# Kernel optimization log

Measured on AMD Instinct MI355X. Metric: run time of the kernel, lower is better.

The kernel has to match this reference:

```python
import jax, jax.numpy as jnp
import numpy as np

D = 1024      # model_dim (input_dim)
H = 2048      # hidden_size_per_expert (hardcoded in module)
E = 8         # num_experts
K = 2         # topk
T = 8192      # tokens (batch after view)


def setup_inputs() -> dict:
    key = jax.random.key(0)
    ks = jax.random.split(key, 6)
    s_in = 1.0 / np.sqrt(D)
    s_h = 1.0 / np.sqrt(H)
    return {
        "x": jax.random.normal(ks[0], (T, D), dtype=jnp.float32),
        "wg": jax.random.normal(ks[1], (D, E), dtype=jnp.float32) * s_in,   # gate Linear(D,E,bias=False)
        "w1": jax.random.normal(ks[2], (E, D, H), dtype=jnp.float32) * s_in,
        "b1": jnp.zeros((E, H), dtype=jnp.float32),
        "w2": jax.random.normal(ks[3], (E, H, D), dtype=jnp.float32) * s_h,
        "b2": jnp.zeros((E, D), dtype=jnp.float32),
    }


def _moe(x, wg, w1, b1, w2, b2):
    # top-k gating (Tutel 'top' gate, k=K)
    logits = x @ wg                         # [T,E]
    scores = jax.nn.softmax(logits, -1)     # [T,E]
    topv, topi = jax.lax.top_k(scores, K)   # [T,K]
    sel = jax.nn.one_hot(topi, E, dtype=x.dtype)          # [T,K,E]
    combine = jnp.einsum('tk,tke->te', topv, sel)          # sparse combine weights [T,E]
    # GShard-style load-balance aux loss (top-1 dispatch mask)
    ce = sel[:, 0, :].mean(0)               # fraction of tokens whose top1 is e
    me = scores.mean(0)                     # mean gate prob per expert
    l_aux = jnp.sum(me * ce) * E
    # expert FFN (dense over experts; combine zeros out non-selected)
    h = jax.nn.relu(jnp.einsum('td,edh->teh', x, w1) + b1)  # [T,E,H]
    y = jnp.einsum('teh,ehd->ted', h, w2) + b2              # [T,E,D]
    out = jnp.einsum('te,ted->td', combine, y)              # [T,D]
    return out, l_aux


def reference(x, wg, w1, b1, w2, b2):
    return _moe(x, wg, w1, b1, w2, b2)
```

## Files before the change

### kernel.cpp

```cpp
#include <hip/hip_runtime.h>
#include <stdint.h>

#define T_TOK 8192
#define DIM   1024
#define HID   2048
#define NE    8

#define BM 128
#define BN 128
#define BK 64

#define GB_TOK 32

typedef float floatx4 __attribute__((ext_vector_type(4)));
typedef short shortx8 __attribute__((ext_vector_type(8)));

typedef __attribute__((address_space(3))) void       lds_void;
typedef const __attribute__((address_space(1))) void gbl_void;

__device__ __forceinline__ unsigned short f2bf(float f) {
  unsigned int u = __float_as_uint(f);
  unsigned int r = 0x7fffu + ((u >> 16) & 1u);
  return (unsigned short)((u + r) >> 16);
}

__global__ __launch_bounds__(256) void transpose_cast_kernel(const float* __restrict__ in,
                                                             unsigned short* __restrict__ out,
                                                             int R, int C) {
  __shared__ float tile[32][33];
  const size_t eoff = (size_t)blockIdx.z * R * C;
  const float* ip = in + eoff;
  unsigned short* op = out + eoff;
  int c0 = blockIdx.x * 32, r0 = blockIdx.y * 32;
  int tx = threadIdx.x, ty = threadIdx.y;
#pragma unroll
  for (int i = 0; i < 4; i++)
    tile[ty + i * 8][tx] = ip[(size_t)(r0 + ty + i * 8) * C + (c0 + tx)];
  __syncthreads();
#pragma unroll
  for (int i = 0; i < 4; i++)
    op[(size_t)(c0 + ty + i * 8) * R + (r0 + tx)] = f2bf(tile[tx][ty + i * 8]);
}

__global__ __launch_bounds__(256) void gate_kernel(const float* __restrict__ x,
                                                   const float* __restrict__ wg,
                                                   unsigned short* __restrict__ xb,
                                                   int* counts, int* top1cnt, float* ssum,
                                                   int* tok_list, float* wgt_list) {
  __shared__ int   lds_cnt[8];
  __shared__ int   lds_top1[8];
  __shared__ float lds_ssum[4][8];
  __shared__ int   tk_e[GB_TOK][2];
  __shared__ int   tk_r[GB_TOK][2];
  __shared__ float tk_w[GB_TOK][2];
  __shared__ int   base[8];

  const int tid = threadIdx.x;
  const int wave = tid >> 6;
  const int lane = tid & 63;

  if (tid < 8) { lds_cnt[tid] = 0; lds_top1[tid] = 0; }
  if (tid < 32) lds_ssum[tid >> 3][tid & 7] = 0.f;
  __syncthreads();

  float ssum_local[8];
#pragma unroll
  for (int e = 0; e < 8; e++) ssum_local[e] = 0.f;

  for (int it = 0; it < GB_TOK / 4; it++) {
    const int lt = it * 4 + wave;
    const int t = blockIdx.x * GB_TOK + lt;

    float acc[8];
#pragma unroll
    for (int e = 0; e < 8; e++) acc[e] = 0.f;
    const float* xr = x + (size_t)t * DIM;
    unsigned short* xw = xb + (size_t)t * DIM;
#pragma unroll
    for (int i = 0; i < 16; i++) {
      int d = i * 64 + lane;
      float xv = xr[d];
      xw[d] = f2bf(xv);
      const float4* wr = reinterpret_cast<const float4*>(wg + d * 8);
      float4 w0 = wr[0], w1 = wr[1];
      acc[0] += xv * w0.x; acc[1] += xv * w0.y; acc[2] += xv * w0.z; acc[3] += xv * w0.w;
      acc[4] += xv * w1.x; acc[5] += xv * w1.y; acc[6] += xv * w1.z; acc[7] += xv * w1.w;
    }
#pragma unroll
    for (int e = 0; e < 8; e++) {
#pragma unroll
      for (int off = 32; off > 0; off >>= 1) acc[e] += __shfl_xor(acc[e], off, 64);
    }
    if (lane == 0) {
      float mx = acc[0];
#pragma unroll
      for (int e = 1; e < 8; e++) mx = fmaxf(mx, acc[e]);
      float s[8], sum = 0.f;
#pragma unroll
      for (int e = 0; e < 8; e++) { s[e] = expf(acc[e] - mx); sum += s[e]; }
      float inv = 1.f / sum;
#pragma unroll
      for (int e = 0; e < 8; e++) { s[e] *= inv; ssum_local[e] += s[e]; }
      int i1 = 0;
#pragma unroll
      for (int e = 1; e < 8; e++) if (s[e] > s[i1]) i1 = e;
      int i2 = (i1 == 0) ? 1 : 0;
#pragma unroll
      for (int e = 0; e < 8; e++) if (e != i1 && s[e] > s[i2]) i2 = e;
      atomicAdd(&lds_top1[i1], 1);
      int r1 = atomicAdd(&lds_cnt[i1], 1);
      int r2 = atomicAdd(&lds_cnt[i2], 1);
      tk_e[lt][0] = i1; tk_r[lt][0] = r1; tk_w[lt][0] = s[i1];
      tk_e[lt][1] = i2; tk_r[lt][1] = r2; tk_w[lt][1] = s[i2];
    }
  }
  if (lane == 0) {
#pragma unroll
    for (int e = 0; e < 8; e++) lds_ssum[wave][e] = ssum_local[e];
  }
  __syncthreads();
  if (tid < 8) {
    base[tid] = atomicAdd(&counts[tid], lds_cnt[tid]);
    atomicAdd(&top1cnt[tid], lds_top1[tid]);
    atomicAdd(&ssum[tid],
              lds_ssum[0][tid] + lds_ssum[1][tid] + lds_ssum[2][tid] + lds_ssum[3][tid]);
  }
  __syncthreads();
  if (tid < GB_TOK * 2) {
    int lt = tid >> 1, k = tid & 1;
    int e = tk_e[lt][k];
    int pos = base[e] + tk_r[lt][k];
    tok_list[e * T_TOK + pos] = blockIdx.x * GB_TOK + lt;
    wgt_list[e * T_TOK + pos] = tk_w[lt][k];
  }
}

__global__ void scan_kernel(const int* counts, const int* top1cnt, const float* ssum,
                            int* h_off, int* tile_off, float* laux_out) {
  if (threadIdx.x == 0 && blockIdx.x == 0) {
    int off = 0, toff = 0;
    float l = 0.f;
    for (int e = 0; e < 8; e++) {
      h_off[e] = off;
      tile_off[e] = toff;
      off += counts[e];
      toff += (counts[e] + BM - 1) / BM;
      l += (ssum[e] / (float)T_TOK) * ((float)top1cnt[e] / (float)T_TOK);
    }
    tile_off[8] = toff;
    *laux_out = l * (float)NE;
  }
}

template <int MODE>
__global__ __launch_bounds__(256, 2) void moe_gemm_kernel(
    const unsigned short* __restrict__ A_src, const unsigned short* __restrict__ B_src,
    const float* __restrict__ bias, const int* __restrict__ counts,
    const int* __restrict__ h_off, const int* __restrict__ tile_off,
    const int* __restrict__ tok_list, const float* __restrict__ wgt_list,
    unsigned short* __restrict__ h_out, float* __restrict__ out, int N, int K) {
  __shared__ unsigned short s_a[2][BM][BK];
  __shared__ unsigned short s_b[2][BN][BK];

  const int bt = blockIdx.y;
  if (bt >= tile_off[8]) return;
  int e = 7;
#pragma unroll
  for (int q = 6; q >= 0; q--)
    if (bt < tile_off[q + 1]) e = q;
  const int n_e = counts[e];
  const int m0 = (bt - tile_off[e]) * BM;
  const int n0 = blockIdx.x * BN;
  const int tid = threadIdx.x;

  const int lane = tid & 63;
  const int wv = tid >> 6;
  const int lrow = lane >> 3;
  const int lchk = (lane & 7) ^ lrow;

  const unsigned short* a_g[4];
  const unsigned short* b_g[4];
#pragma unroll
  for (int c = 0; c < 4; c++) {
    int ra = wv * 32 + c * 8 + lrow;
    int gr = m0 + ra;
    int safe = (gr < n_e) ? gr : (n_e - 1);
    const unsigned short* abase;
    if (MODE == 0) {
      int tok = tok_list[e * T_TOK + safe];
      abase = A_src + (size_t)tok * K;
    } else {
      abase = A_src + (size_t)(h_off[e] + safe) * K;
    }
    a_g[c] = abase + lchk * 8;
    b_g[c] = B_src + ((size_t)e * N + n0 + ra) * K + lchk * 8;
  }

  auto STAGE = [&](int buf, int kt) {
#pragma unroll
    for (int c = 0; c < 4; c++) {
      __builtin_amdgcn_global_load_lds((gbl_void*)(a_g[c] + kt),
                                       (lds_void*)&s_a[buf][wv * 32 + c * 8][0], 16, 0, 0);
      __builtin_amdgcn_global_load_lds((gbl_void*)(b_g[c] + kt),
                                       (lds_void*)&s_b[buf][wv * 32 + c * 8][0], 16, 0, 0);
    }
  };

  const int lm = lane & 15;
  const int quad = lane >> 4;
  const int r7 = lm & 7;
  const int wm = (wv >> 1) * 64;
  const int wn = (wv & 1) * 64;

  floatx4 acc[4][4];
#pragma unroll
  for (int mi = 0; mi < 4; mi++)
#pragma unroll
    for (int ni = 0; ni < 4; ni++) acc[mi][ni] = (floatx4){0.f, 0.f, 0.f, 0.f};

  const int NT = K / BK;
  STAGE(0, 0);
  __syncthreads();

  int cur = 0;
  for (int t = 0; t < NT; ++t) {
    if (t + 1 < NT) STAGE(cur ^ 1, (t + 1) * BK);
#pragma unroll
    for (int kk = 0; kk < 2; kk++) {
      const int pc = ((kk << 2) + quad) ^ r7;
      shortx8 af[4], bfr[4];
#pragma unroll
      for (int mi = 0; mi < 4; mi++)
        af[mi] = *reinterpret_cast<const shortx8*>(&s_a[cur][wm + mi * 16 + lm][pc << 3]);
#pragma unroll
      for (int ni = 0; ni < 4; ni++)
        bfr[ni] = *reinterpret_cast<const shortx8*>(&s_b[cur][wn + ni * 16 + lm][pc << 3]);
#pragma unroll
      for (int mi = 0; mi < 4; mi++)
#pragma unroll
        for (int ni = 0; ni < 4; ni++)
          acc[mi][ni] = __builtin_amdgcn_mfma_f32_16x16x32_bf16(af[mi], bfr[ni], acc[mi][ni], 0, 0, 0);
    }
    __syncthreads();
    cur ^= 1;
  }

#pragma unroll
  for (int mi = 0; mi < 4; mi++) {
#pragma unroll
    for (int r = 0; r < 4; r++) {
      int row = m0 + wm + mi * 16 + quad * 4 + r;
      if (row >= n_e) continue;
      if (MODE == 0) {
        size_t base = (size_t)(h_off[e] + row) * N;
#pragma unroll
        for (int ni = 0; ni < 4; ni++) {
          int col = n0 + wn + ni * 16 + lm;
          float v = acc[mi][ni][r] + bias[e * N + col];
          v = fmaxf(v, 0.f);
          h_out[base + col] = f2bf(v);
        }
      } else {
        int tok = tok_list[e * T_TOK + row];
        float wgt = wgt_list[e * T_TOK + row];
        size_t base = (size_t)tok * N;
#pragma unroll
        for (int ni = 0; ni < 4; ni++) {
          int col = n0 + wn + ni * 16 + lm;
          float v = wgt * (acc[mi][ni][r] + bias[e * N + col]);
          atomicAdd(&out[base + col], v);
        }
      }
    }
  }
}

extern "C" void kernel_launch(void* const* d_in, const int* in_sizes, int n_in,
                              void* d_out, int out_size, void* d_ws, size_t ws_size,
                              hipStream_t stream) {
  const float* x  = (const float*)d_in[0];
  const float* wg = (const float*)d_in[1];
  const float* w1 = (const float*)d_in[2];
  const float* b1 = (const float*)d_in[3];
  const float* w2 = (const float*)d_in[4];
  const float* b2 = (const float*)d_in[5];
  float* out = (float*)d_out;

  char* ws = (char*)d_ws;
  int*            counts   = (int*)(ws + 0);
  int*            top1cnt  = (int*)(ws + 32);
  float*          ssum     = (float*)(ws + 64);
  int*            h_off    = (int*)(ws + 96);
  int*            tile_off = (int*)(ws + 128);
  int*            tok_list = (int*)(ws + 256);
  float*          wgt_list = (float*)(ws + 262400);
  unsigned short* x_bf     = (unsigned short*)(ws + 524544);
  unsigned short* w1t      = (unsigned short*)(ws + 17301760);
  unsigned short* w2t      = (unsigned short*)(ws + 50856192);
  unsigned short* h_buf    = (unsigned short*)(ws + 84410624);

  hipMemsetAsync(ws, 0, 256, stream);
  hipMemsetAsync(d_out, 0, (size_t)out_size * sizeof(float), stream);

  dim3 tb(32, 8);
  transpose_cast_kernel<<<dim3(HID / 32, DIM / 32, NE), tb, 0, stream>>>(w1, w1t, DIM, HID);
  transpose_cast_kernel<<<dim3(DIM / 32, HID / 32, NE), tb, 0, stream>>>(w2, w2t, HID, DIM);

  gate_kernel<<<T_TOK / GB_TOK, 256, 0, stream>>>(x, wg, x_bf, counts, top1cnt, ssum,
                                                  tok_list, wgt_list);
  scan_kernel<<<1, 64, 0, stream>>>(counts, top1cnt, ssum, h_off, tile_off,
                                    out + (size_t)T_TOK * DIM);

  moe_gemm_kernel<0><<<dim3(HID / BN, 136, 1), 256, 0, stream>>>(
      x_bf, w1t, b1, counts, h_off, tile_off, tok_list, wgt_list, h_buf, nullptr, HID, DIM);
  moe_gemm_kernel<1><<<dim3(DIM / BN, 136, 1), 256, 0, stream>>>(
      h_buf, w2t, b2, counts, h_off, tile_off, tok_list, wgt_list, nullptr, out, DIM, HID);
}
```

Measured before the change: 539.9 us.

## Single-buffer LDS, raise occupancy, and remap 1D grid for XCD-aware tile order

Drops the LDS double buffer in favor of single-buffered load-then-compute with two barriers per K step, halving LDS use so launch bounds can request 4 blocks per CU. It also flattens the grid to 1D and remaps block ids so consecutive blocks on the same XCD (bid&7) walk contiguous tile rows, improving L2 reuse of A/B tiles. The cost is that global loads are no longer overlapped with MFMA inside a block, and the kernel relies on other resident blocks to hide that latency. Register pressure under the 4-block bound may also force spills.

```diff
diff --git a/kernel.cpp b/kernel.cpp
--- a/kernel.cpp
+++ b/kernel.cpp
@@ -153,16 +153,22 @@
 }
 
 template <int MODE>
-__global__ __launch_bounds__(256, 2) void moe_gemm_kernel(
+__global__ __launch_bounds__(256, 4) void moe_gemm_kernel(
     const unsigned short* __restrict__ A_src, const unsigned short* __restrict__ B_src,
     const float* __restrict__ bias, const int* __restrict__ counts,
     const int* __restrict__ h_off, const int* __restrict__ tile_off,
     const int* __restrict__ tok_list, const float* __restrict__ wgt_list,
     unsigned short* __restrict__ h_out, float* __restrict__ out, int N, int K) {
-  __shared__ unsigned short s_a[2][BM][BK];
-  __shared__ unsigned short s_b[2][BN][BK];
-
-  const int bt = blockIdx.y;
+  __shared__ unsigned short s_a[BM][BK];
+  __shared__ unsigned short s_b[BN][BK];
+
+  const int ntx = N / BN;
+  const int cpx = ntx * 17;
+  const int bid = blockIdx.x;
+  const int wg  = (bid & 7) * cpx + (bid >> 3);
+  const int bt  = wg / ntx;
+  const int nt  = wg - bt * ntx;
+
   if (bt >= tile_off[8]) return;
   int e = 7;
 #pragma unroll
@@ -170,7 +176,7 @@
     if (bt < tile_off[q + 1]) e = q;
   const int n_e = counts[e];
   const int m0 = (bt - tile_off[e]) * BM;
-  const int n0 = blockIdx.x * BN;
+  const int n0 = nt * BN;
   const int tid = threadIdx.x;
 
   const int lane = tid & 63;
@@ -180,6 +186,8 @@
 
   const unsigned short* a_g[4];
   const unsigned short* b_g[4];
+  lds_void* a_l[4];
+  lds_void* b_l[4];
 #pragma unroll
   for (int c = 0; c < 4; c++) {
     int ra = wv * 32 + c * 8 + lrow;
@@ -194,17 +202,9 @@
     }
     a_g[c] = abase + lchk * 8;
     b_g[c] = B_src + ((size_t)e * N + n0 + ra) * K + lchk * 8;
-  }
-
-  auto STAGE = [&](int buf, int kt) {
-#pragma unroll
-    for (int c = 0; c < 4; c++) {
-      __builtin_amdgcn_global_load_lds((gbl_void*)(a_g[c] + kt),
-                                       (lds_void*)&s_a[buf][wv * 32 + c * 8][0], 16, 0, 0);
-      __builtin_amdgcn_global_load_lds((gbl_void*)(b_g[c] + kt),
-                                       (lds_void*)&s_b[buf][wv * 32 + c * 8][0], 16, 0, 0);
-    }
-  };
+    a_l[c] = (lds_void*)&s_a[wv * 32 + c * 8][0];
+    b_l[c] = (lds_void*)&s_b[wv * 32 + c * 8][0];
+  }
 
   const int lm = lane & 15;
   const int quad = lane >> 4;
@@ -218,23 +218,23 @@
 #pragma unroll
     for (int ni = 0; ni < 4; ni++) acc[mi][ni] = (floatx4){0.f, 0.f, 0.f, 0.f};
 
-  const int NT = K / BK;
-  STAGE(0, 0);
-  __syncthreads();
-
-  int cur = 0;
-  for (int t = 0; t < NT; ++t) {
-    if (t + 1 < NT) STAGE(cur ^ 1, (t + 1) * BK);
+  for (int kt = 0; kt < K; kt += BK) {
+#pragma unroll
+    for (int c = 0; c < 4; c++) {
+      __builtin_amdgcn_global_load_lds((gbl_void*)(a_g[c] + kt), a_l[c], 16, 0, 0);
+      __builtin_amdgcn_global_load_lds((gbl_void*)(b_g[c] + kt), b_l[c], 16, 0, 0);
+    }
+    __syncthreads();
 #pragma unroll
     for (int kk = 0; kk < 2; kk++) {
       const int pc = ((kk << 2) + quad) ^ r7;
       shortx8 af[4], bfr[4];
 #pragma unroll
       for (int mi = 0; mi < 4; mi++)
-        af[mi] = *reinterpret_cast<const shortx8*>(&s_a[cur][wm + mi * 16 + lm][pc << 3]);
+        af[mi] = *reinterpret_cast<const shortx8*>(&s_a[wm + mi * 16 + lm][pc << 3]);
 #pragma unroll
       for (int ni = 0; ni < 4; ni++)
-        bfr[ni] = *reinterpret_cast<const shortx8*>(&s_b[cur][wn + ni * 16 + lm][pc << 3]);
+        bfr[ni] = *reinterpret_cast<const shortx8*>(&s_b[wn + ni * 16 + lm][pc << 3]);
 #pragma unroll
       for (int mi = 0; mi < 4; mi++)
 #pragma unroll
@@ -242,7 +242,6 @@
           acc[mi][ni] = __builtin_amdgcn_mfma_f32_16x16x32_bf16(af[mi], bfr[ni], acc[mi][ni], 0, 0, 0);
     }
     __syncthreads();
-    cur ^= 1;
   }
 
 #pragma unroll
@@ -311,8 +310,8 @@
   scan_kernel<<<1, 64, 0, stream>>>(counts, top1cnt, ssum, h_off, tile_off,
                                     out + (size_t)T_TOK * DIM);
 
-  moe_gemm_kernel<0><<<dim3(HID / BN, 136, 1), 256, 0, stream>>>(
+  moe_gemm_kernel<0><<<dim3((HID / BN) * 136), 256, 0, stream>>>(
       x_bf, w1t, b1, counts, h_off, tile_off, tok_list, wgt_list, h_buf, nullptr, HID, DIM);
-  moe_gemm_kernel<1><<<dim3(DIM / BN, 136, 1), 256, 0, stream>>>(
+  moe_gemm_kernel<1><<<dim3((DIM / BN) * 136), 256, 0, stream>>>(
       h_buf, w2t, b2, counts, h_off, tile_off, tok_list, wgt_list, nullptr, out, DIM, HID);
 }
```

Measured after the change: 461.1 us. 1.17x faster.
